# Kernel optimization log

Measured on AMD Instinct MI355X. Metric: run time of the kernel, lower is better.

## Reference

```python
import jax, jax.numpy as jnp
import numpy as np

C = 1.0
TAU = 1.0
LE = 1.0
LH = 1.0
LN_EPS = 1e-5

def _safe_norm(x, keepdims=False):
    return jnp.clip(jnp.sqrt(jnp.sum(x * x, axis=-1, keepdims=keepdims)), 1e-15)

def _project_to_ball(x, c, eps=1e-5):
    sqrt_c = c ** 0.5
    norm = _safe_norm(x, keepdims=True)
    max_norm = (1.0 - eps) / sqrt_c
    scale = jnp.where(norm > max_norm, max_norm / norm, 1.0)
    return x * scale

def _lambda_x(x, c):
    x = _project_to_ball(x, c)
    x2 = jnp.sum(x * x, axis=-1, keepdims=True)
    return 2.0 / jnp.clip(1.0 - c * x2, 1e-15)

def _mobius_add(x, y, c):
    x = _project_to_ball(x, c)
    y = _project_to_ball(y, c)
    x2 = jnp.sum(x * x, axis=-1, keepdims=True)
    y2 = jnp.sum(y * y, axis=-1, keepdims=True)
    xy = jnp.sum(x * y, axis=-1, keepdims=True)
    num = (1 + 2 * c * xy + c * y2) * x + (1 - c * x2) * y
    den = 1 + 2 * c * xy + c ** 2 * x2 * y2
    return num / jnp.clip(den, 1e-15)

def _exp_map_x(x, v, c):
    sqrt_c = c ** 0.5
    lam = _lambda_x(x, c)
    vnorm = _safe_norm(v, keepdims=True)
    v_dir = v / vnorm
    factor = jnp.tanh(lam * sqrt_c * vnorm / 2.0) / sqrt_c
    out = _mobius_add(x, v_dir * factor, c)
    return _project_to_ball(out, c)

def _log_map_x(x, y, c):
    sqrt_c = c ** 0.5
    lam = _lambda_x(x, c)
    u = _mobius_add(-x, y, c)
    unorm = _safe_norm(u, keepdims=True)
    u_dir = u / unorm
    arg = jnp.minimum(sqrt_c * unorm, 1 - 1e-7)
    scale = 2.0 / (lam * sqrt_c) * jnp.arctanh(arg)
    return scale * u_dir

def _poincare_distance_sq(x, y, c):
    sqrt_c = c ** 0.5
    x = _project_to_ball(x, c)
    y = _project_to_ball(y, c)
    diff = _mobius_add(-x, y, c)
    norm = _safe_norm(diff, keepdims=False)
    arg = jnp.minimum(sqrt_c * norm, 1 - 1e-7)
    dist = 2.0 / sqrt_c * jnp.arctanh(arg)
    return dist * dist

def setup_inputs() -> dict:
    key = jax.random.key(0)
    ks = jax.random.split(key, 6)
    B, N, L, A, de, dh, z_dim = 8, 8, 64, 64, 128, 64, 128
    z_e, z_h = z_dim // 2 + z_dim % 2, z_dim // 2
    return {
        "curr_rho_batch": jax.random.normal(ks[0], (B, A, de), jnp.float32),
        "curr_hyp_emb": 0.1 * jax.random.normal(ks[1], (B, dh), jnp.float32),
        "demo_rho_batch": jax.random.normal(ks[2], (B, N, L, A, de), jnp.float32),
        "demo_hyp_emb": 0.1 * jax.random.normal(ks[3], (B, N, L, dh), jnp.float32),
        "We": 0.02 * jax.random.normal(ks[4], (z_e, de), jnp.float32),
        "Wh": 0.02 * jax.random.normal(ks[5], (z_h, dh), jnp.float32),
        "ln_gamma": jnp.ones((z_dim,), jnp.float32),
        "ln_beta": jnp.zeros((z_dim,), jnp.float32),
    }

def reference(curr_rho_batch, curr_hyp_emb, demo_rho_batch, demo_hyp_emb, We, Wh, ln_gamma, ln_beta):
    B, A, de = curr_rho_batch.shape
    _, N, L, _, _ = demo_rho_batch.shape
    M = N * L
    dh = curr_hyp_emb.shape[-1]
    demo_rho_flat = demo_rho_batch.reshape(B, M, A, de)   # [B,M,A,de]
    demo_hyp_flat = demo_hyp_emb.reshape(B, M, dh)        # [B,M,dh]
    # Euclidean squared distances: [B,M,A] -> [B,A,M]
    e_diff_sq = jnp.sum((curr_rho_batch[:, None, :, :] - demo_rho_flat) ** 2, axis=-1)
    e_diff_sq = jnp.transpose(e_diff_sq, (0, 2, 1))
    # Hyperbolic squared distances: [B,M]
    dH2 = _poincare_distance_sq(curr_hyp_emb[:, None, :], demo_hyp_flat, C)
    scores = -(LH * dH2[:, None, :] + LE * e_diff_sq) / max(TAU, 1e-8)  # [B,A,M]
    alpha = jax.nn.softmax(scores, axis=-1)
    # Euclidean aggregation
    e_out = jnp.einsum('bam,bmad->bad', alpha, demo_rho_flat)  # [B,A,de]
    # Hyperbolic Karcher-mean step
    log_vecs = _log_map_x(curr_hyp_emb[:, None, :], demo_hyp_flat, C)  # [B,M,dh]
    v = jnp.einsum('bam,bmd->bad', alpha, log_vecs)  # [B,A,dh]
    x_ba = jnp.broadcast_to(curr_hyp_emb[:, None, :], (B, A, dh))
    h_out = _exp_map_x(x_ba, v, C)  # [B,A,dh]
    z = jnp.concatenate([e_out @ We.T, h_out @ Wh.T], axis=-1)  # [B,A,z_dim]
    mean = jnp.mean(z, axis=-1, keepdims=True)
    var = jnp.var(z, axis=-1, keepdims=True)
    z = (z - mean) / jnp.sqrt(var + LN_EPS) * ln_gamma + ln_beta
    return z
```

## Files before the change

kernel.cpp:

```cpp
#include <hip/hip_runtime.h>

#define DEV __device__ __forceinline__

constexpr int A_ = 64, DE = 128, M_ = 512;

DEV float wred_sum64(float v) {
#pragma unroll
    for (int o = 1; o < 64; o <<= 1) v += __shfl_xor(v, o, 64);
    return v;
}

__global__ __launch_bounds__(256) void k_hyp(const float* __restrict__ curr_hyp,
                                             const float* __restrict__ demo_hyp,
                                             float* __restrict__ dH2,
                                             float* __restrict__ logv) {
    const int lane = threadIdx.x & 63;
    const int r    = (blockIdx.x << 2) + (threadIdx.x >> 6);
    const int b    = r >> 9;

    float x = curr_hyp[(b << 6) + lane];
    float y = demo_hyp[((size_t)r << 6) + lane];
    const float mx = 1.0f - 1e-5f;

    float x2r = wred_sum64(x * x);
    float xn  = fmaxf(sqrtf(x2r), 1e-15f);
    float sx  = xn > mx ? mx / xn : 1.0f;
    x *= sx;
    float x2 = x2r * sx * sx;
    float y2r = wred_sum64(y * y);
    float yn  = fmaxf(sqrtf(y2r), 1e-15f);
    float sy  = yn > mx ? mx / yn : 1.0f;
    y *= sy;
    float y2 = y2r * sy * sy;

    float xy = wred_sum64(x * y);
    float num = (1.f - 2.f * xy + y2) * (-x) + (1.f - x2) * y;
    float den = fmaxf(1.f - 2.f * xy + x2 * y2, 1e-15f);
    float u   = num / den;

    float u2  = wred_sum64(u * u);
    float un  = fmaxf(sqrtf(u2), 1e-15f);
    float arg = fminf(un, 1.f - 1e-7f);
    float at  = 0.5f * __logf((1.f + arg) / (1.f - arg));

    if (lane == 0) dH2[r] = 4.f * at * at;

    float lamden = fmaxf(1.f - x2, 1e-15f);
    float ls     = lamden * at / un;
    logv[((size_t)r << 6) + lane] = ls * u;
}

__global__ __launch_bounds__(256) void k_attn(const float* __restrict__ curr_rho,
                                              const float* __restrict__ demo_rho,
                                              const float* __restrict__ dH2,
                                              float* __restrict__ alpha_ws,
                                              float* __restrict__ eout_ws) {
    __shared__ __align__(16) float lds_k[64 * 132];
    __shared__ float lds_scores[512];
    __shared__ float redmax[4];
    __shared__ float redsum[4];

    const int t    = threadIdx.x;
    const int lane = t & 63;
    const int wv   = t >> 6;
    const int dp   = t & 15;
    const int mi   = t >> 4;
    const int blk  = blockIdx.x;
    const int b    = blk >> 6, a = blk & 63;

    float qf[8];
    {
        float4 q0 = *(const float4*)(curr_rho + (size_t)blk * DE + dp * 8);
        float4 q1 = *(const float4*)(curr_rho + (size_t)blk * DE + dp * 8 + 4);
        qf[0] = q0.x; qf[1] = q0.y; qf[2] = q0.z; qf[3] = q0.w;
        qf[4] = q1.x; qf[5] = q1.y; qf[6] = q1.z; qf[7] = q1.w;
    }
    float e_acc[8];
#pragma unroll
    for (int j = 0; j < 8; j++) e_acc[j] = 0.f;
    float gmax = -1e30f, gsum = 0.f;

    const size_t rowStride = (size_t)A_ * DE;

    for (int c = 0; c < 8; c++) {
        __syncthreads();
        const float* dbase = demo_rho + ((size_t)(b * M_ + c * 64) * A_ + a) * DE;
#pragma unroll
        for (int p = 0; p < 8; p++) {
            int unit = p * 256 + t;
            int row = unit >> 5, part = unit & 31;
            float4 v = *(const float4*)(dbase + (size_t)row * rowStride + part * 4);
            *(float4*)(&lds_k[row * 132 + part * 4]) = v;
        }
        __syncthreads();

        float sc[4], kf[4][8];
        float lmax = -1e30f;
#pragma unroll
        for (int s = 0; s < 4; s++) {
            const int m = mi * 4 + s;
            float4 k0 = *(const float4*)(&lds_k[m * 132 + dp * 8]);
            float4 k1 = *(const float4*)(&lds_k[m * 132 + dp * 8 + 4]);
            kf[s][0] = k0.x; kf[s][1] = k0.y; kf[s][2] = k0.z; kf[s][3] = k0.w;
            kf[s][4] = k1.x; kf[s][5] = k1.y; kf[s][6] = k1.z; kf[s][7] = k1.w;
            float part = 0.f;
#pragma unroll
            for (int j = 0; j < 8; j++) { float d = qf[j] - kf[s][j]; part += d * d; }
            part += __shfl_xor(part, 1, 64);
            part += __shfl_xor(part, 2, 64);
            part += __shfl_xor(part, 4, 64);
            part += __shfl_xor(part, 8, 64);
            float dv = dH2[b * M_ + c * 64 + m];
            sc[s] = -(dv + part);
            lmax  = fmaxf(lmax, sc[s]);
            if (dp == 0) lds_scores[c * 64 + m] = sc[s];
        }
        lmax = fmaxf(lmax, __shfl_xor(lmax, 16, 64));
        lmax = fmaxf(lmax, __shfl_xor(lmax, 32, 64));
        if (lane == 0) redmax[wv] = lmax;
        __syncthreads();
        float cmax = fmaxf(fmaxf(redmax[0], redmax[1]), fmaxf(redmax[2], redmax[3]));
        float gnew = fmaxf(gmax, cmax);
        float resc = __expf(gmax - gnew);
        gmax = gnew;
        gsum *= resc;
#pragma unroll
        for (int j = 0; j < 8; j++) e_acc[j] *= resc;

        float w[4];
        float wsum = 0.f;
#pragma unroll
        for (int s = 0; s < 4; s++) { w[s] = __expf(sc[s] - gmax); wsum += w[s]; }
        wsum += __shfl_xor(wsum, 16, 64);
        wsum += __shfl_xor(wsum, 32, 64);
        if (lane == 0) redsum[wv] = wsum;
#pragma unroll
        for (int s = 0; s < 4; s++)
#pragma unroll
            for (int j = 0; j < 8; j++) e_acc[j] = fmaf(w[s], kf[s][j], e_acc[j]);
        __syncthreads();
        gsum += redsum[0] + redsum[1] + redsum[2] + redsum[3];
    }

    const float inv = 1.f / gsum;
    for (int i = t; i < 512; i += 256)
        alpha_ws[(size_t)blk * 512 + i] = __expf(lds_scores[i] - gmax) * inv;
    float* rede = (float*)lds_k;
    *(float4*)&rede[mi * 132 + dp * 8]     = make_float4(e_acc[0], e_acc[1], e_acc[2], e_acc[3]);
    *(float4*)&rede[mi * 132 + dp * 8 + 4] = make_float4(e_acc[4], e_acc[5], e_acc[6], e_acc[7]);
    __syncthreads();
    if (t < 128) {
        float s = 0.f;
#pragma unroll
        for (int g = 0; g < 16; g++) s += rede[g * 132 + t];
        eout_ws[(size_t)blk * 128 + t] = s * inv;
    }
}

__global__ __launch_bounds__(256) void k_final(const float* __restrict__ curr_hyp,
                                               const float* __restrict__ alpha_ws,
                                               const float* __restrict__ logv,
                                               const float* __restrict__ eout_ws,
                                               const float* __restrict__ We,
                                               const float* __restrict__ Wh,
                                               const float* __restrict__ gamma,
                                               const float* __restrict__ beta,
                                               float* __restrict__ out) {
    __shared__ float vpart[4][64];
    __shared__ float eh[192];
    const int t = threadIdx.x, w = t >> 6, lane = t & 63;
    const int blk = blockIdx.x, b = blk >> 6;

    const float* arow = alpha_ws + (size_t)blk * 512;
    const float* lvb  = logv + (size_t)b * 512 * 64;
    float acc = 0.f;
#pragma unroll 8
    for (int m = w * 128; m < w * 128 + 128; ++m)
        acc = fmaf(arow[m], lvb[(size_t)m * 64 + lane], acc);
    vpart[w][lane] = acc;
    __syncthreads();

    if (w == 0) {
        float v = vpart[0][lane] + vpart[1][lane] + vpart[2][lane] + vpart[3][lane];
        const float mx = 1.0f - 1e-5f;
        float x = curr_hyp[(b << 6) + lane];
        float x2r = wred_sum64(x * x);
        float xn  = fmaxf(sqrtf(x2r), 1e-15f);
        float sx  = xn > mx ? mx / xn : 1.f;
        x *= sx;
        float x2 = x2r * sx * sx;
        float lamden = fmaxf(1.f - x2, 1e-15f);

        float v2 = wred_sum64(v * v);
        float vn = fmaxf(sqrtf(v2), 1e-15f);
        float targ   = vn / lamden;
        float e2     = __expf(2.f * targ);
        float factor = 1.f - 2.f / (e2 + 1.f);
        float wvv    = v * (factor / vn);

        float w2 = wred_sum64(wvv * wvv);
        float xw = wred_sum64(x * wvv);
        float num = (1.f + 2.f * xw + w2) * x + (1.f - x2) * wvv;
        float den = fmaxf(1.f + 2.f * xw + x2 * w2, 1e-15f);
        float h   = num / den;
        float h2  = wred_sum64(h * h);
        float hn  = fmaxf(sqrtf(h2), 1e-15f);
        float shh = hn > mx ? mx / hn : 1.f;
        h *= shh;

        eh[lane]       = eout_ws[(size_t)blk * 128 + lane];
        eh[64 + lane]  = eout_ws[(size_t)blk * 128 + 64 + lane];
        eh[128 + lane] = h;
    }
    __syncthreads();

    if (w == 0) {
        float ze = 0.f;
        const float* werow = We + lane * 128;
#pragma unroll
        for (int d0 = 0; d0 < 128; d0 += 4) {
            float4 wv4 = *(const float4*)(werow + d0);
            ze = fmaf(eh[d0 + 0], wv4.x, ze);
            ze = fmaf(eh[d0 + 1], wv4.y, ze);
            ze = fmaf(eh[d0 + 2], wv4.z, ze);
            ze = fmaf(eh[d0 + 3], wv4.w, ze);
        }
        float zh = 0.f;
        const float* whrow = Wh + lane * 64;
#pragma unroll
        for (int d0 = 0; d0 < 64; d0 += 4) {
            float4 wv4 = *(const float4*)(whrow + d0);
            zh = fmaf(eh[128 + d0 + 0], wv4.x, zh);
            zh = fmaf(eh[128 + d0 + 1], wv4.y, zh);
            zh = fmaf(eh[128 + d0 + 2], wv4.z, zh);
            zh = fmaf(eh[128 + d0 + 3], wv4.w, zh);
        }
        float ssum = wred_sum64(ze + zh);
        float mean = ssum * (1.f / 128.f);
        float sq   = wred_sum64(ze * ze + zh * zh);
        float var  = sq * (1.f / 128.f) - mean * mean;
        float rinv = rsqrtf(var + 1e-5f);
        float oe = (ze - mean) * rinv * gamma[lane] + beta[lane];
        float oh = (zh - mean) * rinv * gamma[64 + lane] + beta[64 + lane];
        out[(size_t)blk * 128 + lane]      = oe;
        out[(size_t)blk * 128 + 64 + lane] = oh;
    }
}

extern "C" void kernel_launch(void* const* d_in, const int* in_sizes, int n_in,
                              void* d_out, int out_size, void* d_ws, size_t ws_size,
                              hipStream_t stream) {
    const float* curr_rho = (const float*)d_in[0];
    const float* curr_hyp = (const float*)d_in[1];
    const float* demo_rho = (const float*)d_in[2];
    const float* demo_hyp = (const float*)d_in[3];
    const float* We       = (const float*)d_in[4];
    const float* Wh       = (const float*)d_in[5];
    const float* gamma    = (const float*)d_in[6];
    const float* beta     = (const float*)d_in[7];
    float* out = (float*)d_out;

    float* ws    = (float*)d_ws;
    float* dH2   = ws;
    float* logv  = ws + 4096;
    float* alpha = ws + 4096 + 262144;
    float* eout  = ws + 4096 + 2 * 262144;

    k_hyp<<<1024, 256, 0, stream>>>(curr_hyp, demo_hyp, dH2, logv);
    k_attn<<<512, 256, 0, stream>>>(curr_rho, demo_rho, dH2, alpha, eout);
    k_final<<<512, 256, 0, stream>>>(curr_hyp, alpha, logv, eout, We, Wh, gamma, beta, out);
}
```

Before: 219.1 us.

## Fuse attention and final projection kernels with double-buffered demo_rho prefetch

Merges the attention kernel and the final aggregation/projection kernel into one 512-thread block per (b,a). The alpha and e_out intermediates stay in shared memory instead of making a global round-trip, and one kernel launch is removed. The demo_rho rows are now streamed in 32-row chunks through two shared buffers, with the next chunk loaded into registers before the current one is processed. The online softmax is restructured so each of the 8 waves combines its own max and sum per chunk. The costs are higher register and LDS pressure at 512 threads and more barrier rounds, since there are 16 chunks instead of 8.

Result: faster. 211.7 us (-3.4%).

```diff
diff --git a/kernel.cpp b/kernel.cpp
--- a/kernel.cpp
+++ b/kernel.cpp
@@ -2,7 +2,7 @@
 
 #define DEV __device__ __forceinline__
 
-constexpr int A_ = 64, DE = 128, M_ = 512;
+constexpr int A_ = 64, DE = 128, M_ = 512, DH = 64;
 
 DEV float wred_sum64(float v) {
 #pragma unroll
@@ -50,15 +50,23 @@
     logv[((size_t)r << 6) + lane] = ls * u;
 }
 
-__global__ __launch_bounds__(256) void k_attn(const float* __restrict__ curr_rho,
-                                              const float* __restrict__ demo_rho,
-                                              const float* __restrict__ dH2,
-                                              float* __restrict__ alpha_ws,
-                                              float* __restrict__ eout_ws) {
-    __shared__ __align__(16) float lds_k[64 * 132];
-    __shared__ float lds_scores[512];
-    __shared__ float redmax[4];
-    __shared__ float redsum[4];
+__global__ __launch_bounds__(512, 4) void k_main(const float* __restrict__ curr_rho,
+                                                 const float* __restrict__ demo_rho,
+                                                 const float* __restrict__ curr_hyp,
+                                                 const float* __restrict__ dH2,
+                                                 const float* __restrict__ logv,
+                                                 const float* __restrict__ We,
+                                                 const float* __restrict__ Wh,
+                                                 const float* __restrict__ gamma,
+                                                 const float* __restrict__ beta,
+                                                 float* __restrict__ out) {
+    __shared__ __align__(16) float buf[2][32 * 132];
+    __shared__ float lds_sc[512];
+    __shared__ float lds_dh[512];
+    __shared__ float redmax[8];
+    __shared__ float redsum[8];
+    __shared__ float vpart[8][64];
+    __shared__ float eh[192];
 
     const int t    = threadIdx.x;
     const int lane = t & 63;
@@ -68,6 +76,8 @@
     const int blk  = blockIdx.x;
     const int b    = blk >> 6, a = blk & 63;
 
+    lds_dh[t] = dH2[(b << 9) + t];
+
     float qf[8];
     {
         float4 q0 = *(const float4*)(curr_rho + (size_t)blk * DE + dp * 8);
@@ -75,113 +85,109 @@
         qf[0] = q0.x; qf[1] = q0.y; qf[2] = q0.z; qf[3] = q0.w;
         qf[4] = q1.x; qf[5] = q1.y; qf[6] = q1.z; qf[7] = q1.w;
     }
+
+    const size_t rowStride = (size_t)A_ * DE;
+    const float* base_ba = demo_rho + ((size_t)b * M_ * A_ + a) * DE;
+    const int r0 = t >> 5, part = t & 31;
+
+    {
+        float4 s0 = *(const float4*)(base_ba + (size_t)r0 * rowStride + part * 4);
+        float4 s1 = *(const float4*)(base_ba + (size_t)(r0 + 16) * rowStride + part * 4);
+        *(float4*)&buf[0][r0 * 132 + part * 4]        = s0;
+        *(float4*)&buf[0][(r0 + 16) * 132 + part * 4] = s1;
+    }
+
     float e_acc[8];
 #pragma unroll
     for (int j = 0; j < 8; j++) e_acc[j] = 0.f;
     float gmax = -1e30f, gsum = 0.f;
 
-    const size_t rowStride = (size_t)A_ * DE;
-
-    for (int c = 0; c < 8; c++) {
+    for (int c = 0; c < 16; ++c) {
+        const int cur = c & 1;
+        float4 n0, n1;
+        if (c < 15) {
+            const float* dbase = base_ba + (size_t)(c + 1) * 32 * rowStride;
+            n0 = *(const float4*)(dbase + (size_t)r0 * rowStride + part * 4);
+            n1 = *(const float4*)(dbase + (size_t)(r0 + 16) * rowStride + part * 4);
+        }
         __syncthreads();
-        const float* dbase = demo_rho + ((size_t)(b * M_ + c * 64) * A_ + a) * DE;
-#pragma unroll
-        for (int p = 0; p < 8; p++) {
-            int unit = p * 256 + t;
-            int row = unit >> 5, part = unit & 31;
-            float4 v = *(const float4*)(dbase + (size_t)row * rowStride + part * 4);
-            *(float4*)(&lds_k[row * 132 + part * 4]) = v;
-        }
+
+        float kf[8];
+        {
+            float4 k0 = *(const float4*)&buf[cur][mi * 132 + dp * 8];
+            float4 k1 = *(const float4*)&buf[cur][mi * 132 + dp * 8 + 4];
+            kf[0] = k0.x; kf[1] = k0.y; kf[2] = k0.z; kf[3] = k0.w;
+            kf[4] = k1.x; kf[5] = k1.y; kf[6] = k1.z; kf[7] = k1.w;
+        }
+        float ps = 0.f;
+#pragma unroll
+        for (int j = 0; j < 8; j++) { float d = qf[j] - kf[j]; ps += d * d; }
+        ps += __shfl_xor(ps, 1, 64);
+        ps += __shfl_xor(ps, 2, 64);
+        ps += __shfl_xor(ps, 4, 64);
+        ps += __shfl_xor(ps, 8, 64);
+        float sc = -(lds_dh[c * 32 + mi] + ps);
+        if (dp == 0) lds_sc[c * 32 + mi] = sc;
+
+        float lm = fmaxf(sc, __shfl_xor(sc, 16, 64));
+        lm = fmaxf(lm, __shfl_xor(lm, 32, 64));
+        float wexp = __expf(sc - lm);
+        float wsum = wexp + __shfl_xor(wexp, 16, 64);
+        wsum += __shfl_xor(wsum, 32, 64);
+        if (lane == 0) { redmax[wv] = lm; redsum[wv] = wsum; }
         __syncthreads();
 
-        float sc[4], kf[4][8];
-        float lmax = -1e30f;
-#pragma unroll
-        for (int s = 0; s < 4; s++) {
-            const int m = mi * 4 + s;
-            float4 k0 = *(const float4*)(&lds_k[m * 132 + dp * 8]);
-            float4 k1 = *(const float4*)(&lds_k[m * 132 + dp * 8 + 4]);
-            kf[s][0] = k0.x; kf[s][1] = k0.y; kf[s][2] = k0.z; kf[s][3] = k0.w;
-            kf[s][4] = k1.x; kf[s][5] = k1.y; kf[s][6] = k1.z; kf[s][7] = k1.w;
-            float part = 0.f;
-#pragma unroll
-            for (int j = 0; j < 8; j++) { float d = qf[j] - kf[s][j]; part += d * d; }
-            part += __shfl_xor(part, 1, 64);
-            part += __shfl_xor(part, 2, 64);
-            part += __shfl_xor(part, 4, 64);
-            part += __shfl_xor(part, 8, 64);
-            float dv = dH2[b * M_ + c * 64 + m];
-            sc[s] = -(dv + part);
-            lmax  = fmaxf(lmax, sc[s]);
-            if (dp == 0) lds_scores[c * 64 + m] = sc[s];
-        }
-        lmax = fmaxf(lmax, __shfl_xor(lmax, 16, 64));
-        lmax = fmaxf(lmax, __shfl_xor(lmax, 32, 64));
-        if (lane == 0) redmax[wv] = lmax;
-        __syncthreads();
-        float cmax = fmaxf(fmaxf(redmax[0], redmax[1]), fmaxf(redmax[2], redmax[3]));
+        float cmax = redmax[0];
+#pragma unroll
+        for (int w = 1; w < 8; w++) cmax = fmaxf(cmax, redmax[w]);
+        float csum = 0.f;
+#pragma unroll
+        for (int w = 0; w < 8; w++) csum += redsum[w] * __expf(redmax[w] - cmax);
         float gnew = fmaxf(gmax, cmax);
-        float resc = __expf(gmax - gnew);
+        float r1 = __expf(gmax - gnew);
+        float r2 = __expf(cmax - gnew);
+        gsum = gsum * r1 + csum * r2;
+        float w = __expf(sc - gnew);
+#pragma unroll
+        for (int j = 0; j < 8; j++) e_acc[j] = fmaf(w, kf[j], e_acc[j] * r1);
         gmax = gnew;
-        gsum *= resc;
-#pragma unroll
-        for (int j = 0; j < 8; j++) e_acc[j] *= resc;
-
-        float w[4];
-        float wsum = 0.f;
-#pragma unroll
-        for (int s = 0; s < 4; s++) { w[s] = __expf(sc[s] - gmax); wsum += w[s]; }
-        wsum += __shfl_xor(wsum, 16, 64);
-        wsum += __shfl_xor(wsum, 32, 64);
-        if (lane == 0) redsum[wv] = wsum;
-#pragma unroll
-        for (int s = 0; s < 4; s++)
-#pragma unroll
-            for (int j = 0; j < 8; j++) e_acc[j] = fmaf(w[s], kf[s][j], e_acc[j]);
-        __syncthreads();
-        gsum += redsum[0] + redsum[1] + redsum[2] + redsum[3];
+
+        if (c < 15) {
+            *(float4*)&buf[cur ^ 1][r0 * 132 + part * 4]        = n0;
+            *(float4*)&buf[cur ^ 1][(r0 + 16) * 132 + part * 4] = n1;
+        }
     }
 
     const float inv = 1.f / gsum;
-    for (int i = t; i < 512; i += 256)
-        alpha_ws[(size_t)blk * 512 + i] = __expf(lds_scores[i] - gmax) * inv;
-    float* rede = (float*)lds_k;
+    float al = __expf(lds_sc[t] - gmax) * inv;
+    lds_sc[t] = al;
+
+    float* rede = buf[0];
     *(float4*)&rede[mi * 132 + dp * 8]     = make_float4(e_acc[0], e_acc[1], e_acc[2], e_acc[3]);
     *(float4*)&rede[mi * 132 + dp * 8 + 4] = make_float4(e_acc[4], e_acc[5], e_acc[6], e_acc[7]);
     __syncthreads();
     if (t < 128) {
         float s = 0.f;
 #pragma unroll
-        for (int g = 0; g < 16; g++) s += rede[g * 132 + t];
-        eout_ws[(size_t)blk * 128 + t] = s * inv;
-    }
-}
-
-__global__ __launch_bounds__(256) void k_final(const float* __restrict__ curr_hyp,
-                                               const float* __restrict__ alpha_ws,
-                                               const float* __restrict__ logv,
-                                               const float* __restrict__ eout_ws,
-                                               const float* __restrict__ We,
-                                               const float* __restrict__ Wh,
-                                               const float* __restrict__ gamma,
-                                               const float* __restrict__ beta,
-                                               float* __restrict__ out) {
-    __shared__ float vpart[4][64];
-    __shared__ float eh[192];
-    const int t = threadIdx.x, w = t >> 6, lane = t & 63;
-    const int blk = blockIdx.x, b = blk >> 6;
-
-    const float* arow = alpha_ws + (size_t)blk * 512;
-    const float* lvb  = logv + (size_t)b * 512 * 64;
-    float acc = 0.f;
+        for (int g = 0; g < 32; g++) s += rede[g * 132 + t];
+        eh[t] = s * inv;
+    }
+
+    {
+        const float* lvb = logv + ((size_t)(b * M_) + wv * 64) * DH;
+        float acc = 0.f;
 #pragma unroll 8
-    for (int m = w * 128; m < w * 128 + 128; ++m)
-        acc = fmaf(arow[m], lvb[(size_t)m * 64 + lane], acc);
-    vpart[w][lane] = acc;
+        for (int i = 0; i < 64; ++i)
+            acc = fmaf(lds_sc[wv * 64 + i], lvb[(size_t)i * DH + lane], acc);
+        vpart[wv][lane] = acc;
+    }
     __syncthreads();
 
-    if (w == 0) {
-        float v = vpart[0][lane] + vpart[1][lane] + vpart[2][lane] + vpart[3][lane];
+    if (wv == 0) {
+        float v = 0.f;
+#pragma unroll
+        for (int w = 0; w < 8; w++) v += vpart[w][lane];
+
         const float mx = 1.0f - 1e-5f;
         float x = curr_hyp[(b << 6) + lane];
         float x2r = wred_sum64(x * x);
@@ -207,14 +213,8 @@
         float hn  = fmaxf(sqrtf(h2), 1e-15f);
         float shh = hn > mx ? mx / hn : 1.f;
         h *= shh;
-
-        eh[lane]       = eout_ws[(size_t)blk * 128 + lane];
-        eh[64 + lane]  = eout_ws[(size_t)blk * 128 + 64 + lane];
         eh[128 + lane] = h;
-    }
-    __syncthreads();
-
-    if (w == 0) {
+
         float ze = 0.f;
         const float* werow = We + lane * 128;
 #pragma unroll
@@ -260,13 +260,11 @@
     const float* beta     = (const float*)d_in[7];
     float* out = (float*)d_out;
 
-    float* ws    = (float*)d_ws;
-    float* dH2   = ws;
-    float* logv  = ws + 4096;
-    float* alpha = ws + 4096 + 262144;
-    float* eout  = ws + 4096 + 2 * 262144;
+    float* ws   = (float*)d_ws;
+    float* dH2  = ws;
+    float* logv = ws + 4096;
 
     k_hyp<<<1024, 256, 0, stream>>>(curr_hyp, demo_hyp, dH2, logv);
-    k_attn<<<512, 256, 0, stream>>>(curr_rho, demo_rho, dH2, alpha, eout);
-    k_final<<<512, 256, 0, stream>>>(curr_hyp, alpha, logv, eout, We, Wh, gamma, beta, out);
-}
+    k_main<<<512, 512, 0, stream>>>(curr_rho, demo_rho, curr_hyp, dH2, logv,
+                                    We, Wh, gamma, beta, out);
+}
```
